# Performance work log

Measured on AMD Instinct MI355X. Metric: run time of the kernel, lower is better.

The kernel has to match this reference:

```python
import jax, jax.numpy as jnp
import numpy as np

N_NODES = 100000
NUM_FEATURES = 64
HIDDEN = 128
OUT_CONV2 = 100


def gcn_conv(x, W, b, src, dst, n):
    """PyG GCNConv: add self-loops, symmetric degree norm, scatter-add."""
    x = x @ W  # [N, out]
    loop = jnp.arange(n, dtype=src.dtype)
    src2 = jnp.concatenate([src, loop])  # [E+N]
    dst2 = jnp.concatenate([dst, loop])
    deg = jax.ops.segment_sum(jnp.ones_like(dst2, dtype=x.dtype), dst2, num_segments=n)
    dinv = jnp.where(deg > 0, deg ** -0.5, 0.0)
    norm = dinv[src2] * dinv[dst2]  # [E+N]
    msg = x[src2] * norm[:, None]  # gather + scale
    out = jax.ops.segment_sum(msg, dst2, num_segments=n)  # scatter-add
    return out + b


def setup_inputs() -> dict:
    key = jax.random.key(0)
    ks = jax.random.split(key, 8)
    E = 1600000
    x = jax.random.normal(ks[0], (N_NODES, NUM_FEATURES), dtype=jnp.float32)
    edge_index = jax.random.randint(ks[1], (2, E), 0, N_NODES, dtype=jnp.int64)
    # Glorot-style init for GCNConv weights, zeros bias (PyG defaults)
    s1 = (6.0 / (NUM_FEATURES + HIDDEN)) ** 0.5
    W1 = jax.random.uniform(ks[2], (NUM_FEATURES, HIDDEN), minval=-s1, maxval=s1, dtype=jnp.float32)
    b1 = jnp.zeros((HIDDEN,), dtype=jnp.float32)
    s2 = (6.0 / (HIDDEN + OUT_CONV2)) ** 0.5
    W2 = jax.random.uniform(ks[3], (HIDDEN, OUT_CONV2), minval=-s2, maxval=s2, dtype=jnp.float32)
    b2 = jnp.zeros((OUT_CONV2,), dtype=jnp.float32)
    sl = (1.0 / OUT_CONV2) ** 0.5
    Wl = jax.random.uniform(ks[4], (OUT_CONV2, 1), minval=-sl, maxval=sl, dtype=jnp.float32)
    bl = jax.random.uniform(ks[5], (1,), minval=-sl, maxval=sl, dtype=jnp.float32)
    return {"x": x, "edge_index": edge_index, "W1": W1, "b1": b1,
            "W2": W2, "b2": b2, "Wl": Wl, "bl": bl}


def reference(x, edge_index, W1, b1, W2, b2, Wl, bl):
    src, dst = edge_index[0], edge_index[1]
    h = gcn_conv(x, W1, b1, src, dst, N_NODES)
    h = jax.nn.relu(h)
    # F.dropout with training=False (eval/inference) is identity
    h = gcn_conv(h, W2, b2, src, dst, N_NODES)
    return h @ Wl + bl  # [N, 1]
```

## Files before the change

kernel.cpp:

```cpp
#include <hip/hip_runtime.h>
#include <hip/hip_fp16.h>


#define N_NODES 100000
#define F_IN 64
#define HID 128
#define OUT2 100
#define BSHIFT 7
#define BNODES 128
#define NBUCKETS ((N_NODES + BNODES - 1) / BNODES)
#define SCAP 2560
#define ACHUNK 4096
#define NB_PAD 1024
#define SENTB 0xFFFFu
#define SENTE 0xFFFFFFFFu
#define TSHIFT 13
#define NTILES 13
#define RSTRIDE 77
#define ZROW N_NODES
#define YSCALE 4096.0f
#define YINV   (1.0f / 4096.0f)
#define ZSCALE 8192.0f
#define ZINV   (1.0f / 8192.0f)

typedef _Float16 half8 __attribute__((ext_vector_type(8)));
typedef float f32x4 __attribute__((ext_vector_type(4)));

static __device__ __forceinline__ half8 as_half8(uint4 u) {
    union { uint4 u; half8 h; } x; x.u = u; return x.h;
}

__global__ __launch_bounds__(256) void partA_kernel(
    const int* __restrict__ src, const int* __restrict__ dst,
    int* __restrict__ bcur, unsigned int* __restrict__ ebuf, int E, int nchunks,
    const float* __restrict__ W1, const float* __restrict__ W2,
    const float* __restrict__ b2, const float* __restrict__ Wl,
    const float* __restrict__ bl,
    float* __restrict__ v, float* __restrict__ c, uint4* __restrict__ Wpk,
    int* __restrict__ yzero) {
    int t = threadIdx.x;
    if ((int)blockIdx.x >= nchunks) {
        int pb = (int)blockIdx.x - nchunks;
        if (pb < 8) {
            int idx = pb * 256 + t;
            int lane2 = idx & 63;
            int kf    = (idx >> 6) & 1;
            int cb    = (idx >> 7) & 7;
            int part  = (idx >> 10) & 1;
            union { uint4 u; unsigned short s[8]; } pk;
            #pragma unroll
            for (int j = 0; j < 8; ++j) {
                int k    = kf * 32 + (lane2 >> 4) * 8 + j;
                int colg = cb * 16 + (lane2 & 15);
                float w = W1[k * HID + colg];
                __half h = __float2half_rn(w);
                if (part) h = __float2half_rn(w - __half2float(h));
                pk.s[j] = __half_as_ushort(h);
            }
            Wpk[idx] = pk.u;
        } else {
            if (t < HID) {
                float acc = 0.f;
                for (int k = 0; k < OUT2; ++k) acc += W2[t * OUT2 + k] * Wl[k];
                v[t] = acc;
            } else if (t == HID) {
                float acc = bl[0];
                for (int k = 0; k < OUT2; ++k) acc += b2[k] * Wl[k];
                *c = acc;
            }
            if (t < 128) yzero[t] = 0;
        }
        return;
    }
    __shared__ unsigned int stage[ACHUNK];
    __shared__ unsigned short sb[ACHUNK];
    __shared__ int hist[NB_PAD];
    __shared__ int ocnt[NB_PAD];
    __shared__ int gbase[NB_PAD];
    __shared__ int cnt2[NB_PAD];
    int base = blockIdx.x * ACHUNK;
    int total = E - base; if (total > ACHUNK) total = ACHUNK;

    #pragma unroll
    for (int i = 0; i < 4; ++i) { hist[t + i * 256] = 0; cnt2[t + i * 256] = 0; }
    __syncthreads();

    unsigned int pe[16];
    unsigned short bk[16];
    #pragma unroll
    for (int k = 0; k < 16; ++k) {
        int e = base + k * 256 + t;
        if (e < E) {
            int s = src[e], d = dst[e];
            pe[k] = ((unsigned int)s << BSHIFT) | (unsigned int)(d & (BNODES - 1));
            bk[k] = (unsigned short)(d >> BSHIFT);
            atomicAdd(&hist[bk[k]], 1);
        } else {
            bk[k] = SENTB;
        }
    }
    __syncthreads();
    #pragma unroll
    for (int i = 0; i < 4; ++i) ocnt[t + i * 256] = hist[t + i * 256];
    __syncthreads();
    for (int off = 1; off < NB_PAD; off <<= 1) {
        int v4[4];
        #pragma unroll
        for (int i = 0; i < 4; ++i) {
            int p = t + i * 256;
            v4[i] = (p >= off) ? hist[p - off] : 0;
        }
        __syncthreads();
        #pragma unroll
        for (int i = 0; i < 4; ++i) hist[t + i * 256] += v4[i];
        __syncthreads();
    }
    #pragma unroll
    for (int i = 0; i < 4; ++i) {
        int b = (t + i * 256 + blockIdx.x * 131) & (NB_PAD - 1);
        int cc = ocnt[b];
        if (cc > 0 && b < NBUCKETS)
            gbase[b] = b * SCAP + atomicAdd(&bcur[b], cc);
    }
    __syncthreads();
    #pragma unroll
    for (int k = 0; k < 16; ++k) {
        if (bk[k] != SENTB) {
            int b = bk[k];
            int pos = (hist[b] - ocnt[b]) + atomicAdd(&cnt2[b], 1);
            stage[pos] = pe[k];
            sb[pos] = (unsigned short)b;
        }
    }
    __syncthreads();
    #pragma unroll
    for (int k = 0; k < 16; ++k) {
        int idx = k * 256 + t;
        if (idx < total) {
            int b = sb[idx];
            int lo = hist[b] - ocnt[b];
            ebuf[gbase[b] + (idx - lo)] = stage[idx];
        }
    }
}

__global__ __launch_bounds__(256) void partB_kernel(
    const int* __restrict__ bcur, unsigned int* __restrict__ csr,
    float* __restrict__ dinv,
    const float4* __restrict__ x4, uint2* __restrict__ y2, int n) {
    __shared__ int lcnt[BNODES];
    __shared__ float sdinv[BNODES];
    __shared__ int tcnt[16];
    __shared__ int tcur[16];
    __shared__ unsigned int sbuf[SCAP];
    int b = blockIdx.x, t = threadIdx.x;
    int node0 = b << BSHIFT;
    int nlocal = min(BNODES, n - node0);
    int base = b * SCAP;
    int cnt = bcur[b];
    if (t < BNODES) lcnt[t] = 0;
    if (t < 16) tcnt[t] = 0;
    __syncthreads();
    unsigned int er[SCAP / 256];
    #pragma unroll
    for (int k = 0; k < SCAP / 256; ++k) {
        int idx = k * 256 + t;
        er[k] = (idx < cnt) ? csr[base + idx] : SENTE;
        if (er[k] != SENTE) {
            atomicAdd(&lcnt[er[k] & (BNODES - 1)], 1);
            atomicAdd(&tcnt[er[k] >> (BSHIFT + TSHIFT)], 1);
        }
    }
    __syncthreads();
    if (t < BNODES) {
        float sd = rsqrtf((float)lcnt[t] + 1.0f);
        sdinv[t] = sd;
        if (t < nlocal) dinv[node0 + t] = sd;
    }
    if (t == 0) {
        int s = 0;
        #pragma unroll
        for (int i = 0; i < NTILES; ++i) { tcur[i] = s; s += tcnt[i]; }
    }
    __syncthreads();
    #pragma unroll
    for (int k = 0; k < SCAP / 256; ++k) {
        unsigned int e = er[k];
        if (e != SENTE) {
            int p = atomicAdd(&tcur[e >> (BSHIFT + TSHIFT)], 1);
            sbuf[p] = e;
        }
    }
    __syncthreads();
    for (int idx = t; idx < cnt; idx += 256) csr[base + idx] = sbuf[idx];
    for (int i = t; i < nlocal * 16; i += 256) {
        int nl = i >> 4;
        int gi = (node0 + nl) * 16 + (i & 15);
        float sc = sdinv[nl] * YSCALE;
        float4 xv = x4[gi];
        int a0 = __float2int_rn(xv.x * sc);
        int a1 = __float2int_rn(xv.y * sc);
        int a2 = __float2int_rn(xv.z * sc);
        int a3 = __float2int_rn(xv.w * sc);
        uint2 pk;
        pk.x = ((unsigned int)a0 & 0xFFFFu) | ((unsigned int)a1 << 16);
        pk.y = ((unsigned int)a2 & 0xFFFFu) | ((unsigned int)a3 << 16);
        y2[gi] = pk;
    }
}

#define F1_ISSUE(EE, U, DL)                                            \
    _Pragma("unroll")                                                  \
    for (int g = 0; g < 8; ++g) {                                      \
        unsigned int e_ = __shfl((EE), g * 8 + q, 64);                 \
        int srow_ = (e_ != SENTE) ? (int)(e_ >> BSHIFT) : ZROW;        \
        DL[g] = (int)(e_ & (BNODES - 1));                              \
        U[g] = y4[srow_ * 8 + col];                                    \
    }

#define F1_CONSUME(U, DL)                                              \
    _Pragma("unroll")                                                  \
    for (int g = 0; g < 8; ++g) {                                      \
        int* rowp_ = &acci[DL[g] * RSTRIDE + col * 9];                 \
        const int* up_ = (const int*)&U[g];                            \
        _Pragma("unroll")                                              \
        for (int j = 0; j < 4; ++j) {                                  \
            int d_ = up_[j];                                           \
            atomicAdd(&rowp_[2 * j],     (d_ << 16) >> 16);            \
            atomicAdd(&rowp_[2 * j + 1], d_ >> 16);                    \
        }                                                              \
    }

__global__ __launch_bounds__(256, 4) void fused1_kernel(
    const int4* __restrict__ y4, const short* __restrict__ yh,
    const unsigned int* __restrict__ csr, const int* __restrict__ bcur,
    const float* __restrict__ dinv, const uint4* __restrict__ Wpk,
    const float* __restrict__ b1, const float* __restrict__ v,
    float* __restrict__ zz, int n) {
    __shared__ int acci[BNODES * RSTRIDE];
    int t = threadIdx.x;
    int lane = t & 63, wave = t >> 6;
    int q = lane >> 3, col = lane & 7;
    int b = blockIdx.x;
    int node0 = b << BSHIFT;
    int nlocal = min(BNODES, n - node0);
    int base = b * SCAP;
    int cnt = bcur[b];

    for (int r = wave; r < BNODES; r += 4) {
        int vv = 0;
        if (r < nlocal) vv = (int)yh[(node0 + r) * 64 + lane];
        acci[r * RSTRIDE + (lane >> 3) * 9 + (lane & 7)] = vv;
    }
    __syncthreads();

    int nr = (cnt + 255) >> 8;
    int lpos = wave * 64 + lane;
    unsigned int eeA = (lpos < cnt) ? csr[base + lpos] : SENTE;
    int4 uA[8]; int dlA[8];
    F1_ISSUE(eeA, uA, dlA);
    unsigned int eeB = (lpos + 256 < cnt) ? csr[base + lpos + 256] : SENTE;
    #pragma unroll 2
    for (int r = 0; r < nr; ++r) {
        int4 uN[8]; int dlN[8];
        F1_ISSUE(eeB, uN, dlN);
        int pn = lpos + (r + 2) * 256;
        eeB = (pn < cnt) ? csr[base + pn] : SENTE;
        F1_CONSUME(uA, dlA);
        #pragma unroll
        for (int g = 0; g < 8; ++g) { uA[g] = uN[g]; dlA[g] = dlN[g]; }
    }
    __syncthreads();

    int mm = lane & 15, kq = lane >> 4;
    for (int i = 0; i < 2; ++i) {
        int st = wave * 2 + i;
        int row = st * 16 + mm;
        float dis = ((row < nlocal) ? dinv[node0 + row] : 0.f) * YINV;
        const int* ap = &acci[row * RSTRIDE];
        half8 A0, A1;
        #pragma unroll
        for (int j = 0; j < 8; ++j) {
            A0[j] = (_Float16)(dis * (float)ap[kq * 9 + j]);
            A1[j] = (_Float16)(dis * (float)ap[(4 + kq) * 9 + j]);
        }
        f32x4 acc[8];
        #pragma unroll
        for (int cb = 0; cb < 8; ++cb) acc[cb] = (f32x4){0.f, 0.f, 0.f, 0.f};
        #pragma unroll
        for (int cb = 0; cb < 8; ++cb) {
            half8 bh0 = as_half8(Wpk[(cb * 2 + 0) * 64 + lane]);
            half8 bh1 = as_half8(Wpk[(cb * 2 + 1) * 64 + lane]);
            half8 bl0 = as_half8(Wpk[1024 + (cb * 2 + 0) * 64 + lane]);
            half8 bl1 = as_half8(Wpk[1024 + (cb * 2 + 1) * 64 + lane]);
            acc[cb] = __builtin_amdgcn_mfma_f32_16x16x32_f16(A0, bh0, acc[cb], 0, 0, 0);
            acc[cb] = __builtin_amdgcn_mfma_f32_16x16x32_f16(A1, bh1, acc[cb], 0, 0, 0);
            acc[cb] = __builtin_amdgcn_mfma_f32_16x16x32_f16(A0, bl0, acc[cb], 0, 0, 0);
            acc[cb] = __builtin_amdgcn_mfma_f32_16x16x32_f16(A1, bl1, acc[cb], 0, 0, 0);
        }
        float zp[4] = {0.f, 0.f, 0.f, 0.f};
        #pragma unroll
        for (int cb = 0; cb < 8; ++cb) {
            int colg = cb * 16 + mm;
            float bb1 = b1[colg], vv = v[colg];
            #pragma unroll
            for (int rr = 0; rr < 4; ++rr) {
                float h = acc[cb][rr] + bb1;
                h = fmaxf(h, 0.f);
                zp[rr] += h * vv;
            }
        }
        #pragma unroll
        for (int off = 1; off < 16; off <<= 1) {
            #pragma unroll
            for (int rr = 0; rr < 4; ++rr) zp[rr] += __shfl_xor(zp[rr], off, 64);
        }
        if (mm == 0) {
            int nb = st * 16 + kq * 4;
            #pragma unroll
            for (int rr = 0; rr < 4; ++rr)
                if (nb + rr < nlocal)
                    zz[node0 + nb + rr] = dinv[node0 + nb + rr] * zp[rr];
        }
    }
}

__global__ __launch_bounds__(256) void out_kernel(
    const int* __restrict__ bcur, const unsigned int* __restrict__ csr,
    const float* __restrict__ dinv, const float* __restrict__ zz,
    const float* __restrict__ c, float* __restrict__ out, int n) {
    __shared__ int acc2[BNODES];
    int b = blockIdx.x, t = threadIdx.x;
    int node0 = b << BSHIFT;
    int nlocal = min(BNODES, n - node0);
    int base = b * SCAP;
    int cnt = bcur[b];
    if (t < BNODES) acc2[t] = 0;
    __syncthreads();
    for (int idx = t; idx < cnt; idx += 256) {
        unsigned int e = csr[base + idx];
        float z = zz[e >> BSHIFT];
        atomicAdd(&acc2[e & (BNODES - 1)], __float2int_rn(z * ZSCALE));
    }
    __syncthreads();
    if (t < nlocal) {
        int node = node0 + t;
        out[node] = c[0] + dinv[node] * ((float)acc2[t] * ZINV + zz[node]);
    }
}

extern "C" void kernel_launch(void* const* d_in, const int* in_sizes, int n_in,
                              void* d_out, int out_size, void* d_ws, size_t ws_size,
                              hipStream_t stream) {
    const float* x  = (const float*)d_in[0];
    const int*   ei = (const int*)d_in[1];
    const float* W1 = (const float*)d_in[2];
    const float* b1 = (const float*)d_in[3];
    const float* W2 = (const float*)d_in[4];
    const float* b2 = (const float*)d_in[5];
    const float* Wl = (const float*)d_in[6];
    const float* bl = (const float*)d_in[7];
    float* out = (float*)d_out;

    int E = in_sizes[1] / 2;
    const int* src = ei;
    const int* dst = ei + E;

    float* ws      = (float*)d_ws;
    float* dinv    = ws;
    float* zz      = dinv + N_NODES;
    float* v       = zz + N_NODES;
    float* c       = v + HID;
    int*   bcur    = (int*)(c + 4);
    int*   csr     = bcur + NB_PAD;
    uint4* Wpk     = (uint4*)(csr + (size_t)NBUCKETS * SCAP);
    short* y       = (short*)((float*)Wpk + 8192);

    int nchunks = (E + ACHUNK - 1) / ACHUNK;

    hipMemsetAsync(bcur, 0, NBUCKETS * sizeof(int), stream);
    partA_kernel<<<nchunks + 9, 256, 0, stream>>>(
        src, dst, bcur, (unsigned int*)csr, E, nchunks,
        W1, W2, b2, Wl, bl, v, c, Wpk, (int*)(y + (size_t)ZROW * 64));
    partB_kernel<<<NBUCKETS, 256, 0, stream>>>(
        bcur, (unsigned int*)csr, dinv, (const float4*)x, (uint2*)y, N_NODES);
    fused1_kernel<<<NBUCKETS, 256, 0, stream>>>(
        (const int4*)y, (const short*)y, (const unsigned int*)csr,
        bcur, dinv, Wpk, b1, v, zz, N_NODES);
    out_kernel<<<NBUCKETS, 256, 0, stream>>>(
        bcur, (const unsigned int*)csr, dinv, zz, c, out, N_NODES);
}
```

Before: 182.4 us.

## Halve destination bucket size to 64 nodes and raise fused1 occupancy

Destination buckets shrink from 128 to 64 nodes, so there are twice as many partitions. The bucket-sort histogram, scan and offset loops are widened to 2048 entries to match. fused1 drops its register-heavy double-buffered gather pipeline for a simpler issue-then-consume loop, and each wave handles one 16-row MFMA tile. Launch bounds go from 4 to 6 blocks per CU, with smaller shared accumulators for more parallelism and occupancy. The cost is less memory-latency hiding in the gather, a longer scan in the bucketing kernel, and more blocks each carrying fixed overhead.

```diff
diff --git a/kernel.cpp b/kernel.cpp
--- a/kernel.cpp
+++ b/kernel.cpp
@@ -6,12 +6,12 @@
 #define F_IN 64
 #define HID 128
 #define OUT2 100
-#define BSHIFT 7
-#define BNODES 128
+#define BSHIFT 6
+#define BNODES 64
 #define NBUCKETS ((N_NODES + BNODES - 1) / BNODES)
-#define SCAP 2560
+#define SCAP 1408
 #define ACHUNK 4096
-#define NB_PAD 1024
+#define NB_PAD 2048
 #define SENTB 0xFFFFu
 #define SENTE 0xFFFFFFFFu
 #define TSHIFT 13
@@ -82,7 +82,7 @@
     int total = E - base; if (total > ACHUNK) total = ACHUNK;
 
     #pragma unroll
-    for (int i = 0; i < 4; ++i) { hist[t + i * 256] = 0; cnt2[t + i * 256] = 0; }
+    for (int i = 0; i < 8; ++i) { hist[t + i * 256] = 0; cnt2[t + i * 256] = 0; }
     __syncthreads();
 
     unsigned int pe[16];
@@ -101,22 +101,22 @@
     }
     __syncthreads();
     #pragma unroll
-    for (int i = 0; i < 4; ++i) ocnt[t + i * 256] = hist[t + i * 256];
+    for (int i = 0; i < 8; ++i) ocnt[t + i * 256] = hist[t + i * 256];
     __syncthreads();
     for (int off = 1; off < NB_PAD; off <<= 1) {
-        int v4[4];
-        #pragma unroll
-        for (int i = 0; i < 4; ++i) {
+        int v8[8];
+        #pragma unroll
+        for (int i = 0; i < 8; ++i) {
             int p = t + i * 256;
-            v4[i] = (p >= off) ? hist[p - off] : 0;
+            v8[i] = (p >= off) ? hist[p - off] : 0;
         }
         __syncthreads();
         #pragma unroll
-        for (int i = 0; i < 4; ++i) hist[t + i * 256] += v4[i];
+        for (int i = 0; i < 8; ++i) hist[t + i * 256] += v8[i];
         __syncthreads();
     }
     #pragma unroll
-    for (int i = 0; i < 4; ++i) {
+    for (int i = 0; i < 8; ++i) {
         int b = (t + i * 256 + blockIdx.x * 131) & (NB_PAD - 1);
         int cc = ocnt[b];
         if (cc > 0 && b < NBUCKETS)
@@ -161,9 +161,9 @@
     if (t < BNODES) lcnt[t] = 0;
     if (t < 16) tcnt[t] = 0;
     __syncthreads();
-    unsigned int er[SCAP / 256];
-    #pragma unroll
-    for (int k = 0; k < SCAP / 256; ++k) {
+    unsigned int er[6];
+    #pragma unroll
+    for (int k = 0; k < 6; ++k) {
         int idx = k * 256 + t;
         er[k] = (idx < cnt) ? csr[base + idx] : SENTE;
         if (er[k] != SENTE) {
@@ -184,7 +184,7 @@
     }
     __syncthreads();
     #pragma unroll
-    for (int k = 0; k < SCAP / 256; ++k) {
+    for (int k = 0; k < 6; ++k) {
         unsigned int e = er[k];
         if (e != SENTE) {
             int p = atomicAdd(&tcur[e >> (BSHIFT + TSHIFT)], 1);
@@ -231,7 +231,7 @@
         }                                                              \
     }
 
-__global__ __launch_bounds__(256, 4) void fused1_kernel(
+__global__ __launch_bounds__(256, 6) void fused1_kernel(
     const int4* __restrict__ y4, const short* __restrict__ yh,
     const unsigned int* __restrict__ csr, const int* __restrict__ bcur,
     const float* __restrict__ dinv, const uint4* __restrict__ Wpk,
@@ -250,78 +250,71 @@
     for (int r = wave; r < BNODES; r += 4) {
         int vv = 0;
         if (r < nlocal) vv = (int)yh[(node0 + r) * 64 + lane];
-        acci[r * RSTRIDE + (lane >> 3) * 9 + (lane & 7)] = vv;
+        acci[r * RSTRIDE + q * 9 + col] = vv;
     }
     __syncthreads();
 
     int nr = (cnt + 255) >> 8;
     int lpos = wave * 64 + lane;
-    unsigned int eeA = (lpos < cnt) ? csr[base + lpos] : SENTE;
-    int4 uA[8]; int dlA[8];
-    F1_ISSUE(eeA, uA, dlA);
-    unsigned int eeB = (lpos + 256 < cnt) ? csr[base + lpos + 256] : SENTE;
-    #pragma unroll 2
+    unsigned int ee = (lpos < cnt) ? csr[base + lpos] : SENTE;
     for (int r = 0; r < nr; ++r) {
-        int4 uN[8]; int dlN[8];
-        F1_ISSUE(eeB, uN, dlN);
-        int pn = lpos + (r + 2) * 256;
-        eeB = (pn < cnt) ? csr[base + pn] : SENTE;
-        F1_CONSUME(uA, dlA);
-        #pragma unroll
-        for (int g = 0; g < 8; ++g) { uA[g] = uN[g]; dlA[g] = dlN[g]; }
+        int pn = lpos + (r + 1) * 256;
+        unsigned int een = (pn < cnt) ? csr[base + pn] : SENTE;
+        int4 u[8]; int dl[8];
+        F1_ISSUE(ee, u, dl);
+        F1_CONSUME(u, dl);
+        ee = een;
     }
     __syncthreads();
 
     int mm = lane & 15, kq = lane >> 4;
-    for (int i = 0; i < 2; ++i) {
-        int st = wave * 2 + i;
-        int row = st * 16 + mm;
-        float dis = ((row < nlocal) ? dinv[node0 + row] : 0.f) * YINV;
-        const int* ap = &acci[row * RSTRIDE];
-        half8 A0, A1;
-        #pragma unroll
-        for (int j = 0; j < 8; ++j) {
-            A0[j] = (_Float16)(dis * (float)ap[kq * 9 + j]);
-            A1[j] = (_Float16)(dis * (float)ap[(4 + kq) * 9 + j]);
-        }
-        f32x4 acc[8];
-        #pragma unroll
-        for (int cb = 0; cb < 8; ++cb) acc[cb] = (f32x4){0.f, 0.f, 0.f, 0.f};
-        #pragma unroll
-        for (int cb = 0; cb < 8; ++cb) {
-            half8 bh0 = as_half8(Wpk[(cb * 2 + 0) * 64 + lane]);
-            half8 bh1 = as_half8(Wpk[(cb * 2 + 1) * 64 + lane]);
-            half8 bl0 = as_half8(Wpk[1024 + (cb * 2 + 0) * 64 + lane]);
-            half8 bl1 = as_half8(Wpk[1024 + (cb * 2 + 1) * 64 + lane]);
-            acc[cb] = __builtin_amdgcn_mfma_f32_16x16x32_f16(A0, bh0, acc[cb], 0, 0, 0);
-            acc[cb] = __builtin_amdgcn_mfma_f32_16x16x32_f16(A1, bh1, acc[cb], 0, 0, 0);
-            acc[cb] = __builtin_amdgcn_mfma_f32_16x16x32_f16(A0, bl0, acc[cb], 0, 0, 0);
-            acc[cb] = __builtin_amdgcn_mfma_f32_16x16x32_f16(A1, bl1, acc[cb], 0, 0, 0);
-        }
-        float zp[4] = {0.f, 0.f, 0.f, 0.f};
-        #pragma unroll
-        for (int cb = 0; cb < 8; ++cb) {
-            int colg = cb * 16 + mm;
-            float bb1 = b1[colg], vv = v[colg];
-            #pragma unroll
-            for (int rr = 0; rr < 4; ++rr) {
-                float h = acc[cb][rr] + bb1;
-                h = fmaxf(h, 0.f);
-                zp[rr] += h * vv;
-            }
-        }
-        #pragma unroll
-        for (int off = 1; off < 16; off <<= 1) {
-            #pragma unroll
-            for (int rr = 0; rr < 4; ++rr) zp[rr] += __shfl_xor(zp[rr], off, 64);
-        }
-        if (mm == 0) {
-            int nb = st * 16 + kq * 4;
-            #pragma unroll
-            for (int rr = 0; rr < 4; ++rr)
-                if (nb + rr < nlocal)
-                    zz[node0 + nb + rr] = dinv[node0 + nb + rr] * zp[rr];
-        }
+    int st = wave;
+    int row = st * 16 + mm;
+    float dis = ((row < nlocal) ? dinv[node0 + row] : 0.f) * YINV;
+    const int* ap = &acci[row * RSTRIDE];
+    half8 A0, A1;
+    #pragma unroll
+    for (int j = 0; j < 8; ++j) {
+        A0[j] = (_Float16)(dis * (float)ap[kq * 9 + j]);
+        A1[j] = (_Float16)(dis * (float)ap[(4 + kq) * 9 + j]);
+    }
+    f32x4 acc[8];
+    #pragma unroll
+    for (int cb = 0; cb < 8; ++cb) acc[cb] = (f32x4){0.f, 0.f, 0.f, 0.f};
+    #pragma unroll
+    for (int cb = 0; cb < 8; ++cb) {
+        half8 bh0 = as_half8(Wpk[(cb * 2 + 0) * 64 + lane]);
+        half8 bh1 = as_half8(Wpk[(cb * 2 + 1) * 64 + lane]);
+        half8 bl0 = as_half8(Wpk[1024 + (cb * 2 + 0) * 64 + lane]);
+        half8 bl1 = as_half8(Wpk[1024 + (cb * 2 + 1) * 64 + lane]);
+        acc[cb] = __builtin_amdgcn_mfma_f32_16x16x32_f16(A0, bh0, acc[cb], 0, 0, 0);
+        acc[cb] = __builtin_amdgcn_mfma_f32_16x16x32_f16(A1, bh1, acc[cb], 0, 0, 0);
+        acc[cb] = __builtin_amdgcn_mfma_f32_16x16x32_f16(A0, bl0, acc[cb], 0, 0, 0);
+        acc[cb] = __builtin_amdgcn_mfma_f32_16x16x32_f16(A1, bl1, acc[cb], 0, 0, 0);
+    }
+    float zp[4] = {0.f, 0.f, 0.f, 0.f};
+    #pragma unroll
+    for (int cb = 0; cb < 8; ++cb) {
+        int colg = cb * 16 + mm;
+        float bb1 = b1[colg], vv = v[colg];
+        #pragma unroll
+        for (int rr = 0; rr < 4; ++rr) {
+            float h = acc[cb][rr] + bb1;
+            h = fmaxf(h, 0.f);
+            zp[rr] += h * vv;
+        }
+    }
+    #pragma unroll
+    for (int off = 1; off < 16; off <<= 1) {
+        #pragma unroll
+        for (int rr = 0; rr < 4; ++rr) zp[rr] += __shfl_xor(zp[rr], off, 64);
+    }
+    if (mm == 0) {
+        int nb = st * 16 + kq * 4;
+        #pragma unroll
+        for (int rr = 0; rr < 4; ++rr)
+            if (nb + rr < nlocal)
+                zz[node0 + nb + rr] = dinv[node0 + nb + rr] * zp[rr];
     }
 }
 
```

Result: no change. 179.2 us (-1.7%).

## Simplify partA bucket scan and drop double-buffered gather pipeline in aggregation

Applied to the files above, without the earlier changes.

Replaces the 1024-element Hillis-Steele scan over bucket histograms with a per-thread 4-element serial scan plus a 256-entry block scan, cutting the number of barrier rounds. In the aggregation kernel, the software-pipelined two-stage prefetch of gathered rows (which held two sets of eight int4 registers) is replaced by a single-stage issue/consume loop with only a one-ahead index prefetch, a sched_barrier and a per-iteration __syncthreads. It also changes the LDS row stride of the accumulator from 77 to 72. The goal is lower register pressure and fewer scan syncs, at the cost of less memory-latency hiding and an extra block barrier per edge round.

```diff
diff --git a/kernel.cpp b/kernel.cpp
--- a/kernel.cpp
+++ b/kernel.cpp
@@ -16,7 +16,7 @@
 #define SENTE 0xFFFFFFFFu
 #define TSHIFT 13
 #define NTILES 13
-#define RSTRIDE 77
+#define RSTRIDE 72
 #define ZROW N_NODES
 #define YSCALE 4096.0f
 #define YINV   (1.0f / 4096.0f)
@@ -78,6 +78,7 @@
     __shared__ int ocnt[NB_PAD];
     __shared__ int gbase[NB_PAD];
     __shared__ int cnt2[NB_PAD];
+    __shared__ int tsum[256];
     int base = blockIdx.x * ACHUNK;
     int total = E - base; if (total > ACHUNK) total = ACHUNK;
 
@@ -103,18 +104,22 @@
     #pragma unroll
     for (int i = 0; i < 4; ++i) ocnt[t + i * 256] = hist[t + i * 256];
     __syncthreads();
-    for (int off = 1; off < NB_PAD; off <<= 1) {
-        int v4[4];
-        #pragma unroll
-        for (int i = 0; i < 4; ++i) {
-            int p = t + i * 256;
-            v4[i] = (p >= off) ? hist[p - off] : 0;
-        }
+    int lcl[4];
+    int s = 0;
+    #pragma unroll
+    for (int i = 0; i < 4; ++i) { s += hist[4 * t + i]; lcl[i] = s; }
+    tsum[t] = s;
+    __syncthreads();
+    for (int off = 1; off < 256; off <<= 1) {
+        int vv = (t >= off) ? tsum[t - off] : 0;
         __syncthreads();
-        #pragma unroll
-        for (int i = 0; i < 4; ++i) hist[t + i * 256] += v4[i];
+        tsum[t] += vv;
         __syncthreads();
     }
+    int cbase = tsum[t] - s;
+    #pragma unroll
+    for (int i = 0; i < 4; ++i) hist[4 * t + i] = cbase + lcl[i];
+    __syncthreads();
     #pragma unroll
     for (int i = 0; i < 4; ++i) {
         int b = (t + i * 256 + blockIdx.x * 131) & (NB_PAD - 1);
@@ -250,25 +255,22 @@
     for (int r = wave; r < BNODES; r += 4) {
         int vv = 0;
         if (r < nlocal) vv = (int)yh[(node0 + r) * 64 + lane];
-        acci[r * RSTRIDE + (lane >> 3) * 9 + (lane & 7)] = vv;
+        acci[r * RSTRIDE + q * 9 + col] = vv;
     }
     __syncthreads();
 
     int nr = (cnt + 255) >> 8;
     int lpos = wave * 64 + lane;
-    unsigned int eeA = (lpos < cnt) ? csr[base + lpos] : SENTE;
-    int4 uA[8]; int dlA[8];
-    F1_ISSUE(eeA, uA, dlA);
-    unsigned int eeB = (lpos + 256 < cnt) ? csr[base + lpos + 256] : SENTE;
-    #pragma unroll 2
+    unsigned int ee = (lpos < cnt) ? csr[base + lpos] : SENTE;
     for (int r = 0; r < nr; ++r) {
-        int4 uN[8]; int dlN[8];
-        F1_ISSUE(eeB, uN, dlN);
-        int pn = lpos + (r + 2) * 256;
-        eeB = (pn < cnt) ? csr[base + pn] : SENTE;
-        F1_CONSUME(uA, dlA);
-        #pragma unroll
-        for (int g = 0; g < 8; ++g) { uA[g] = uN[g]; dlA[g] = dlN[g]; }
+        int pn = lpos + (r + 1) * 256;
+        unsigned int een = (pn < cnt) ? csr[base + pn] : SENTE;
+        int4 u[8]; int dl[8];
+        F1_ISSUE(ee, u, dl);
+        __builtin_amdgcn_sched_barrier(0);
+        F1_CONSUME(u, dl);
+        ee = een;
+        __syncthreads();
     }
     __syncthreads();
 
```

Result: faster. 176.4 us (-3.3%).
